# Kernel optimization log

Hardware: AMD Instinct MI355X
Metric: run time of the kernel (lower is better)

Reference implementation:

```python
import jax, jax.numpy as jnp
import numpy as np

EPS = 1e-6

def setup_inputs() -> dict:
    key = jax.random.key(0)
    k1, k2, k3 = jax.random.split(key, 3)
    B, N, F, OUT = 16, 1024, 64, 128
    x = jax.random.normal(k1, (B, N, F), dtype=jnp.float32)
    A = jax.random.uniform(k2, (B, N, N), dtype=jnp.float32)
    kernel = jax.random.normal(k3, (3 * F, OUT), dtype=jnp.float32) * 0.05
    bias = jnp.zeros((OUT,), dtype=jnp.float32)
    return {"x": x, "A": A, "kernel": kernel, "bias": bias}


def reference(x, A, kernel, bias):
    # x: [B,N,F], A: [B,N,N]
    n = A.shape[-1]
    eye = jnp.eye(n, dtype=A.dtype)
    Az = A * (1.0 - eye)          # zero out diagonal (A -= diag(diag_part(A)))
    A_hat = Az + eye              # add self-loops
    deg = A_hat.sum(axis=2)       # [B,N]
    inv_asym = 1.0 / (EPS + deg)                 # D^{-1}
    s = 1.0 / (EPS + jnp.sqrt(deg))              # D^{-1/2}
    # Three message-passing variants; apply diagonal scalings as broadcasts
    o1 = jnp.matmul(Az, x)                                   # A x
    o2 = inv_asym[:, :, None] * jnp.matmul(A_hat, x)         # D^{-1} A_hat x
    o3 = s[:, :, None] * jnp.matmul(A_hat, s[:, :, None] * x)  # D^{-1/2} A_hat D^{-1/2} x
    out = jnp.concatenate([o1, o2, o3], axis=-1)             # [B,N,3F]
    out = jnp.matmul(out, kernel) + bias                     # [B,N,OUT]
    return jax.nn.relu(out)
```

## Files before the change

kernel.cpp:

```cpp
#include <hip/hip_runtime.h>
#include <hip/hip_bf16.h>
#include <cstdint>

#define NN    1024
#define FF    64
#define OUTF  128
#define KCAT  192
#define EPSV  1e-6f

typedef __attribute__((ext_vector_type(4))) float  f32x4;
typedef __attribute__((ext_vector_type(8))) __bf16 bf16x8;
typedef __attribute__((ext_vector_type(4))) __bf16 bf16x4;

#define MFMA16(a, b, c) __builtin_amdgcn_mfma_f32_16x16x32_bf16(a, b, c, 0, 0, 0)
#define GLOAD_LDS16(g, l)                                          \
    __builtin_amdgcn_global_load_lds(                              \
        (const __attribute__((address_space(1))) void*)(g),        \
        (__attribute__((address_space(3))) void*)(l), 16, 0, 0)

__global__ __launch_bounds__(256) void k_deg_cvt(const float* __restrict__ A,
                                                 float* __restrict__ d1,
                                                 float* __restrict__ sArr,
                                                 __bf16* __restrict__ Az) {
    int wave = threadIdx.x >> 6;
    int lane = threadIdx.x & 63;
    int row  = blockIdx.x * 4 + wave;
    int i    = row & (NN - 1);
    const f32x4* rp = (const f32x4*)(A + (size_t)row * NN);
    __bf16* op = Az + (size_t)row * NN;
    float sum = 0.f;
#pragma unroll
    for (int t = 0; t < 4; ++t) {
        f32x4 v = rp[t * 64 + lane];
        int base = (t * 64 + lane) * 4;
#pragma unroll
        for (int q = 0; q < 4; ++q)
            if (base + q == i) v[q] = 0.f;
        sum += v[0] + v[1] + v[2] + v[3];
        bf16x4 o;
#pragma unroll
        for (int q = 0; q < 4; ++q) o[q] = (__bf16)v[q];
        *(bf16x4*)(op + base) = o;
    }
#pragma unroll
    for (int off = 32; off; off >>= 1) sum += __shfl_xor(sum, off);
    if (lane == 0) {
        float deg = 1.0f + sum;
        d1[row]   = 1.0f / (EPSV + deg);
        sArr[row] = 1.0f / (EPSV + sqrtf(deg));
    }
}

__global__ __launch_bounds__(256) void k_prep(const float* __restrict__ x,
                                              const float* __restrict__ sArr,
                                              const float* __restrict__ kern,
                                              __bf16* __restrict__ xT,
                                              __bf16* __restrict__ sxT,
                                              __bf16* __restrict__ KT) {
    __shared__ float tile[64][65];
    int bid = blockIdx.x;
    int b   = bid >> 4;
    int k0  = (bid & 15) * 64;
    const float* xp = x + ((size_t)b * NN + k0) * FF;
    for (int i = threadIdx.x; i < 64 * 64; i += 256) {
        int r = i >> 6, c = i & 63;
        tile[r][c] = xp[r * FF + c];
    }
    __syncthreads();
    for (int i = threadIdx.x; i < 64 * 64; i += 256) {
        int c = i >> 6, kk = i & 63;
        float v  = tile[kk][c];
        float sv = v * sArr[b * NN + k0 + kk];
        size_t o = ((size_t)b * FF + c) * NN + k0 + kk;
        xT[o]  = (__bf16)v;
        sxT[o] = (__bf16)sv;
    }
    if (threadIdx.x < 96) {
        int idx = bid * 96 + threadIdx.x;
        int c = idx / KCAT;
        int k = idx - c * KCAT;
        KT[idx] = (__bf16)kern[k * OUTF + c];
    }
}

__global__ __launch_bounds__(512, 4) void k_main(const __bf16* __restrict__ Az,
                                                 const float* __restrict__ x,
                                                 const float* __restrict__ bias,
                                                 const float* __restrict__ d1g,
                                                 const float* __restrict__ sg,
                                                 const __bf16* __restrict__ xT,
                                                 const __bf16* __restrict__ sxT,
                                                 const __bf16* __restrict__ KT,
                                                 float* __restrict__ out) {
    __shared__ __align__(16) char smem[81920];

    const int tid  = threadIdx.x;
    const int w    = tid >> 6;
    const int lane = tid & 63;
    const int l15  = lane & 15;
    const int hi   = lane >> 4;
    const int h8   = hi * 8;

    const int idx  = (blockIdx.x & 7) * 64 + (blockIdx.x >> 3);
    const int b    = idx >> 5;
    const int row0 = (idx & 31) * 32;

    const __bf16* AzRow = Az  + (size_t)(b * NN + row0 + (w & 1) * 16 + l15) * NN
                              + (w >> 1) * 32 + h8;
    const __bf16* xRow  = xT  + (size_t)(b * FF + (w & 3) * 16 + l15) * NN
                              + (w >> 2) * 32 + h8;
    const __bf16* sxRow = sxT + (size_t)(b * FF + (w & 3) * 16 + l15) * NN
                              + (w >> 2) * 32 + h8;

#define STAGE(t, pb)                                                     \
    {                                                                    \
        char* bb = smem + (pb) * 40960;                                  \
        const int kofs = (t) * 128;                                      \
        GLOAD_LDS16(AzRow + kofs,      bb + w * 1024);                   \
        GLOAD_LDS16(xRow + kofs,       bb + 8192  + w * 1024);           \
        GLOAD_LDS16(xRow + kofs + 64,  bb + 8192  + (w + 8) * 1024);     \
        GLOAD_LDS16(sxRow + kofs,      bb + 24576 + w * 1024);           \
        GLOAD_LDS16(sxRow + kofs + 64, bb + 24576 + (w + 8) * 1024);     \
    }

    STAGE(0, 0)
    STAGE(1, 1)

    const int rg = w >> 2;
    const int fg = w & 3;

    f32x4 P = {}, Q = {};
#pragma unroll
    for (int t = 0; t < 8; ++t) {
        if (t < 7) { asm volatile("s_waitcnt vmcnt(5)" ::: "memory"); }
        else       { asm volatile("s_waitcnt vmcnt(0)" ::: "memory"); }
        __builtin_amdgcn_s_barrier();
        {
            const char* bb = smem + (t & 1) * 40960;
#pragma unroll
            for (int ks = 0; ks < 4; ++ks) {
                bf16x8 a  = *(const bf16x8*)(bb + (ks * 2 + rg) * 1024 + lane * 16);
                bf16x8 xf = *(const bf16x8*)(bb + 8192  + (ks * 4 + fg) * 1024 + lane * 16);
                bf16x8 sf = *(const bf16x8*)(bb + 24576 + (ks * 4 + fg) * 1024 + lane * 16);
                P = MFMA16(a, xf, P);
                Q = MFMA16(a, sf, Q);
            }
        }
        __builtin_amdgcn_s_barrier();
        if (t < 6) STAGE(t + 2, t & 1)
    }
#undef STAGE

    __bf16 (*os)[216] = (__bf16(*)[216])smem;
#pragma unroll
    for (int j = 0; j < 4; ++j) {
        int rr   = rg * 16 + hi * 4 + j;
        int grow = b * NN + row0 + rr;
        float dv = d1g[grow];
        float sv = sg[grow];
        int cc   = fg * 16 + l15;
        float xv = x[(size_t)grow * FF + cc];
        os[rr][cc]       = (__bf16)P[j];
        os[rr][64 + cc]  = (__bf16)(dv * (P[j] + xv));
        os[rr][128 + cc] = (__bf16)(sv * (Q[j] + sv * xv));
    }
    __syncthreads();

    const int rge = w >> 2;
    const int cge = w & 3;
    f32x4 e0 = {}, e1 = {};
#pragma unroll
    for (int ks = 0; ks < 6; ++ks) {
        bf16x8 of = *(const bf16x8*)&os[rge * 16 + l15][ks * 32 + h8];
        bf16x8 k0 = *(const bf16x8*)&KT[(size_t)(cge * 32 + l15) * KCAT + ks * 32 + h8];
        bf16x8 k1 = *(const bf16x8*)&KT[(size_t)(cge * 32 + 16 + l15) * KCAT + ks * 32 + h8];
        e0 = MFMA16(k0, of, e0);
        e1 = MFMA16(k1, of, e1);
    }
    {
        const size_t orow = (size_t)(b * NN + row0 + rge * 16 + l15) * OUTF;
#pragma unroll
        for (int g = 0; g < 2; ++g) {
            f32x4 ev = g ? e1 : e0;
            int col0 = cge * 32 + g * 16 + hi * 4;
            f32x4 bv = *(const f32x4*)&bias[col0];
            f32x4 rv;
#pragma unroll
            for (int j = 0; j < 4; ++j) {
                float v = ev[j] + bv[j];
                rv[j] = v > 0.f ? v : 0.f;
            }
            *(f32x4*)&out[orow + col0] = rv;
        }
    }
}

extern "C" void kernel_launch(void* const* d_in, const int* in_sizes, int n_in,
                              void* d_out, int out_size, void* d_ws, size_t ws_size,
                              hipStream_t stream) {
    const float* x    = (const float*)d_in[0];
    const float* A    = (const float*)d_in[1];
    const float* kern = (const float*)d_in[2];
    const float* bias = (const float*)d_in[3];
    float* out = (float*)d_out;

    char* ws = (char*)d_ws;
    __bf16* Az  = (__bf16*)(ws);
    float*  d1  = (float*)(ws + 33554432);
    float*  s   = (float*)(ws + 33554432 + 65536);
    __bf16* xT  = (__bf16*)(ws + 33554432 + 131072);
    __bf16* sxT = (__bf16*)(ws + 33554432 + 131072 + 2097152);
    __bf16* KT  = (__bf16*)(ws + 33554432 + 131072 + 2 * 2097152);
    (void)ws_size; (void)in_sizes; (void)n_in; (void)out_size;

    k_deg_cvt<<<dim3(4096), dim3(256), 0, stream>>>(A, d1, s, Az);
    k_prep<<<dim3(256), dim3(256), 0, stream>>>(x, s, kern, xT, sxT, KT);
    k_main<<<dim3(512), dim3(512), 0, stream>>>(Az, x, bias, d1, s, xT, sxT, KT, out);
}
```

Measured before the change: 136.8 us.

## Load full contiguous rows per wave with XOR-swizzled LDS layout in main GEMM

```diff
diff --git a/kernel.cpp b/kernel.cpp
--- a/kernel.cpp
+++ b/kernel.cpp
@@ -105,22 +105,28 @@
     const int b    = idx >> 5;
     const int row0 = (idx & 31) * 32;
 
-    const __bf16* AzRow = Az  + (size_t)(b * NN + row0 + (w & 1) * 16 + l15) * NN
-                              + (w >> 1) * 32 + h8;
-    const __bf16* xRow  = xT  + (size_t)(b * FF + (w & 3) * 16 + l15) * NN
-                              + (w >> 2) * 32 + h8;
-    const __bf16* sxRow = sxT + (size_t)(b * FF + (w & 3) * 16 + l15) * NN
-                              + (w >> 2) * 32 + h8;
+    const int rA = 4 * w + hi;
+    const int sA = (l15 ^ (rA & 7)) * 8;
+    const __bf16* Asrc = Az + (size_t)(b * NN + row0 + rA) * NN + sA;
+
+    const int f0 = 4 * w + hi;
+    const int s0 = (l15 ^ (f0 & 7)) * 8;
+    const int f1 = 32 + 4 * w + hi;
+    const int s1 = (l15 ^ (f1 & 7)) * 8;
+    const __bf16* Xsrc0 = xT  + (size_t)(b * FF + f0) * NN + s0;
+    const __bf16* Xsrc1 = xT  + (size_t)(b * FF + f1) * NN + s1;
+    const __bf16* Ssrc0 = sxT + (size_t)(b * FF + f0) * NN + s0;
+    const __bf16* Ssrc1 = sxT + (size_t)(b * FF + f1) * NN + s1;
 
 #define STAGE(t, pb)                                                     \
     {                                                                    \
         char* bb = smem + (pb) * 40960;                                  \
-        const int kofs = (t) * 128;                                      \
-        GLOAD_LDS16(AzRow + kofs,      bb + w * 1024);                   \
-        GLOAD_LDS16(xRow + kofs,       bb + 8192  + w * 1024);           \
-        GLOAD_LDS16(xRow + kofs + 64,  bb + 8192  + (w + 8) * 1024);     \
-        GLOAD_LDS16(sxRow + kofs,      bb + 24576 + w * 1024);           \
-        GLOAD_LDS16(sxRow + kofs + 64, bb + 24576 + (w + 8) * 1024);     \
+        const int ko = (t) * 128;                                        \
+        GLOAD_LDS16(Asrc + ko,  bb + w * 1024);                          \
+        GLOAD_LDS16(Xsrc0 + ko, bb + 8192  + w * 1024);                  \
+        GLOAD_LDS16(Xsrc1 + ko, bb + 8192  + (w + 8) * 1024);            \
+        GLOAD_LDS16(Ssrc0 + ko, bb + 24576 + w * 1024);                  \
+        GLOAD_LDS16(Ssrc1 + ko, bb + 24576 + (w + 8) * 1024);            \
     }
 
     STAGE(0, 0)
@@ -128,6 +134,13 @@
 
     const int rg = w >> 2;
     const int fg = w & 3;
+
+    const int arow = rg * 16 + l15;
+    const int frow = fg * 16 + l15;
+    const int swz  = (l15 & 7) << 4;
+    const int aBase = arow * 256;
+    const int xBase = 8192 + frow * 256;
+    const int sBase = 24576 + frow * 256;
 
     f32x4 P = {}, Q = {};
 #pragma unroll
@@ -135,17 +148,21 @@
         if (t < 7) { asm volatile("s_waitcnt vmcnt(5)" ::: "memory"); }
         else       { asm volatile("s_waitcnt vmcnt(0)" ::: "memory"); }
         __builtin_amdgcn_s_barrier();
+        __builtin_amdgcn_sched_barrier(0);
         {
             const char* bb = smem + (t & 1) * 40960;
 #pragma unroll
             for (int ks = 0; ks < 4; ++ks) {
-                bf16x8 a  = *(const bf16x8*)(bb + (ks * 2 + rg) * 1024 + lane * 16);
-                bf16x8 xf = *(const bf16x8*)(bb + 8192  + (ks * 4 + fg) * 1024 + lane * 16);
-                bf16x8 sf = *(const bf16x8*)(bb + 24576 + (ks * 4 + fg) * 1024 + lane * 16);
+                const int ko = (ks * 64 + hi * 16) ^ swz;
+                bf16x8 a  = *(const bf16x8*)(bb + aBase + ko);
+                bf16x8 xf = *(const bf16x8*)(bb + xBase + ko);
+                bf16x8 sf = *(const bf16x8*)(bb + sBase + ko);
                 P = MFMA16(a, xf, P);
                 Q = MFMA16(a, sf, Q);
             }
         }
+        asm volatile("s_waitcnt lgkmcnt(0)" ::: "memory");
+        __builtin_amdgcn_sched_barrier(0);
         __builtin_amdgcn_s_barrier();
         if (t < 6) STAGE(t + 2, t & 1)
     }
```

After: 127.0 us. 1.08x faster.
